# Performance work log

Measured on AMD Instinct MI355X. Metric: run time of the kernel, lower is better.

Reference implementation:

```python
import jax, jax.numpy as jnp
import numpy as np

B, P, E = 64, 196, 2048      # batch, num_pixels (14*14), encoder_size
H, EMB, V = 512, 512, 10000  # hidden_size, embed_size, vocab_size
T_CAP = 50                   # hard-coded pred/alpha buffer length
T_MAX = T_CAP - 1            # max(decode_lengths) = max(lengths) - 1 = 49


def setup_inputs() -> dict:
    key = jax.random.key(0)
    ks = jax.random.split(key, 20)

    def lin(k, out_f, in_f):
        kw, kb = jax.random.split(k)
        s = 1.0 / np.sqrt(in_f)
        return (jax.random.uniform(kw, (out_f, in_f), jnp.float32, -s, s),
                jax.random.uniform(kb, (out_f,), jnp.float32, -s, s))

    features = jax.random.normal(ks[0], (B, P, E), jnp.float32)
    captions = jax.random.randint(ks[1], (B, T_CAP), 0, V)
    # sorted descending, first length forced to 50 so max(decode_lengths)=49
    lengths = jnp.sort(jax.random.randint(ks[2], (B,), 2, T_CAP + 1))[::-1]
    lengths = lengths.at[0].set(T_CAP)

    Wx_w, Wx_b = lin(ks[3], E, E)          # attention Wx: encoder->encoder
    Wh_w, Wh_b = lin(ks[4], E, H)          # attention Wh: hidden->encoder
    V_w, V_b = lin(ks[5], 1, E)            # attention V: encoder->1
    init_h_w, init_h_b = lin(ks[6], H, E)  # init_h
    f_beta_w, f_beta_b = lin(ks[7], E, H)  # f_beta gate
    embed_w = jax.random.normal(ks[8], (V, EMB), jnp.float32)
    gru_w_ih, gru_b_ih = lin(ks[9], 3 * H, E + EMB)
    gru_w_hh, gru_b_hh = lin(ks[10], 3 * H, H)
    fc1_w, fc1_b = lin(ks[11], V, H)

    return dict(features=features, captions=captions, lengths=lengths,
                Wx_w=Wx_w, Wx_b=Wx_b, Wh_w=Wh_w, Wh_b=Wh_b, V_w=V_w, V_b=V_b,
                init_h_w=init_h_w, init_h_b=init_h_b,
                f_beta_w=f_beta_w, f_beta_b=f_beta_b, embed_w=embed_w,
                gru_w_ih=gru_w_ih, gru_b_ih=gru_b_ih,
                gru_w_hh=gru_w_hh, gru_b_hh=gru_b_hh,
                fc1_w=fc1_w, fc1_b=fc1_b)


def reference(features, captions, lengths, Wx_w, Wx_b, Wh_w, Wh_b, V_w, V_b,
              init_h_w, init_h_b, f_beta_w, f_beta_b, embed_w,
              gru_w_ih, gru_b_ih, gru_w_hh, gru_b_hh, fc1_w, fc1_b):
    b, p, e = features.shape
    vsz = fc1_w.shape[0]
    dec = lengths - 1                                  # decode_lengths
    # init hidden state from mean-pooled features
    h0 = jnp.mean(features, axis=1) @ init_h_w.T + init_h_b      # [B,H]
    # Wx(features) is time-invariant: precompute once
    x_wx = jnp.einsum('bpe,fe->bpf', features, Wx_w) + Wx_b      # [B,P,E]
    emb = embed_w[captions]                                      # [B,50,EMB]
    emb_t = jnp.transpose(emb[:, :T_MAX], (1, 0, 2))             # [T,B,EMB]

    def step(h, xs):
        t, e_t = xs
        active = (dec >= t)                            # rows still decoding
        # Bahdanau attention
        h_wh = h @ Wh_w.T + Wh_b                       # [B,E]
        lam = jnp.einsum('bpe,oe->bpo',
                         jnp.tanh(x_wx + h_wh[:, None, :]), V_w) + V_b
        alpha = jax.nn.softmax(lam, axis=1)            # [B,P,1]
        z = jnp.sum(alpha * features, axis=1)          # [B,E]
        # sigmoid gate
        gate = jax.nn.sigmoid(h @ f_beta_w.T + f_beta_b)
        inp = jnp.concatenate([gate * z, e_t], axis=1)  # [B,E+EMB]
        # GRUCell (torch gate order r,z,n)
        gi = inp @ gru_w_ih.T + gru_b_ih
        gh = h @ gru_w_hh.T + gru_b_hh
        i_r, i_z, i_n = jnp.split(gi, 3, axis=-1)
        h_r, h_z, h_n = jnp.split(gh, 3, axis=-1)
        r = jax.nn.sigmoid(i_r + h_r)
        zg = jax.nn.sigmoid(i_z + h_z)
        n = jnp.tanh(i_n + r * h_n)
        h_new = (1.0 - zg) * n + zg * h
        pred = h_new @ fc1_w.T + fc1_b                 # dropout in eval = id
        m = active[:, None]
        h_out = jnp.where(m, h_new, h)                 # freeze finished rows
        return h_out, (jnp.where(m, pred, 0.0),
                       jnp.where(m, alpha[..., 0], 0.0))

    _, (preds_t, alphas_t) = jax.lax.scan(
        step, h0, (jnp.arange(T_MAX), emb_t))
    preds = jnp.zeros((b, T_CAP, vsz), features.dtype)
    preds = preds.at[:, :T_MAX].set(jnp.transpose(preds_t, (1, 0, 2)))
    alphas = jnp.zeros((b, T_CAP, p), features.dtype)
    alphas = alphas.at[:, :T_MAX].set(jnp.transpose(alphas_t, (1, 0, 2)))
    return preds, alphas, dec
```

## Files before the change

### kernel.cpp

```cpp
#include <hip/hip_runtime.h>
#include <cstddef>

#define B_    64
#define P_    196
#define E_    2048
#define H_    512
#define EMB_  512
#define V_    10000
#define TCAP_ 50
#define TMAX_ 49
#define KI_   2560
#define G3_   1536
#define NBLK_ 512
#define FSTRIDE 32
#define COLLECTOR_ (NBLK_ - 1)

typedef __attribute__((ext_vector_type(8))) short short8;
typedef __attribute__((ext_vector_type(4))) float floatx4;
typedef unsigned int u32;
typedef __attribute__((ext_vector_type(4))) unsigned int u32x4;
typedef const __attribute__((address_space(1))) u32* gptr_t;
typedef __attribute__((address_space(3))) u32* lptr_t;

__device__ __forceinline__ unsigned short f2bf_rne(float f) {
    unsigned int x = __float_as_uint(f);
    unsigned int r = (x + 0x7fffu + ((x >> 16) & 1u)) >> 16;
    return (unsigned short)r;
}
__device__ __forceinline__ float bf2f(unsigned int u16) {
    return __uint_as_float(u16 << 16);
}
__device__ __forceinline__ float fast_tanh(float x) {
    float a = fabsf(x);
    float e = __expf(2.0f * a);
    float r = 1.0f - 2.0f / (e + 1.0f);
    return (x < 0.0f) ? -r : r;
}
__device__ __forceinline__ float fast_sig(float x) {
    return 1.0f / (1.0f + __expf(-x));
}

__device__ __forceinline__ float ldf(const float* p) {
    return __hip_atomic_load((float*)p, __ATOMIC_RELAXED, __HIP_MEMORY_SCOPE_AGENT);
}
__device__ __forceinline__ void stf(float* p, float v) {
    __hip_atomic_store(p, v, __ATOMIC_RELAXED, __HIP_MEMORY_SCOPE_AGENT);
}
__device__ __forceinline__ void stu(u32* p, u32 v) {
    __hip_atomic_store(p, v, __ATOMIC_RELAXED, __HIP_MEMORY_SCOPE_AGENT);
}
__device__ __forceinline__ short8 cvt8(u32x4 v) {
    union { u32x4 u; short8 s; } x; x.u = v; return x.s;
}

#define GLD16(dst, base, OFF) \
    asm volatile("global_load_dwordx4 %0, %1, off offset:" #OFF " sc1" \
                 : "=v"(dst) : "v"(base) : "memory")

__device__ __forceinline__ void gbar(unsigned int* __restrict__ flags,
                                     unsigned int* __restrict__ go,
                                     unsigned int ep)
{
    asm volatile("s_waitcnt vmcnt(0)" ::: "memory");
    __syncthreads();
    if (blockIdx.x == COLLECTOR_) {
        int tid = threadIdx.x;
        for (int s = tid; s < NBLK_ - 1; s += 256) {
            while (__hip_atomic_load(&flags[s * FSTRIDE], __ATOMIC_RELAXED,
                                     __HIP_MEMORY_SCOPE_AGENT) < ep)
                __builtin_amdgcn_s_sleep(1);
        }
        __syncthreads();
        if (tid < 8)
            __hip_atomic_store(&go[tid * FSTRIDE], ep, __ATOMIC_RELAXED,
                               __HIP_MEMORY_SCOPE_AGENT);
    } else {
        if (threadIdx.x == 0) {
            __hip_atomic_store(&flags[blockIdx.x * FSTRIDE], ep, __ATOMIC_RELAXED,
                               __HIP_MEMORY_SCOPE_AGENT);
            while (__hip_atomic_load(&go[(blockIdx.x & 7) * FSTRIDE], __ATOMIC_RELAXED,
                                     __HIP_MEMORY_SCOPE_AGENT) < ep)
                __builtin_amdgcn_s_sleep(2);
        }
    }
    __syncthreads();
}

__global__ void init_out_kernel(float* __restrict__ preds, float* __restrict__ alphas,
                                float* __restrict__ dec, const int* __restrict__ lens,
                                unsigned int* __restrict__ flags, unsigned int* __restrict__ go)
{
    int i = blockIdx.x * 256 + threadIdx.x;
    if (i < NBLK_ * FSTRIDE) flags[i] = 0u;
    if (i < 8 * FSTRIDE) go[i] = 0u;
    if (i < B_ * V_) {
        int b = i / V_, v = i - b * V_;
        preds[((size_t)b * TCAP_ + TMAX_) * V_ + v] = 0.f;
    }
    if (i < B_ * P_) {
        int b = i / P_, p = i - b * P_;
        alphas[((size_t)b * TCAP_ + TMAX_) * P_ + p] = 0.f;
    }
    if (i < B_) dec[i] = (float)(lens[i] - 1);
}

__global__ void f2bf_kernel(const float* __restrict__ src, unsigned short* __restrict__ dst, int n8)
{
    int i = blockIdx.x * 256 + threadIdx.x;
    if (i >= n8) return;
    float4 a = ((const float4*)src)[2 * i];
    float4 b = ((const float4*)src)[2 * i + 1];
    uint4 o;
    o.x = (unsigned)f2bf_rne(a.x) | ((unsigned)f2bf_rne(a.y) << 16);
    o.y = (unsigned)f2bf_rne(a.z) | ((unsigned)f2bf_rne(a.w) << 16);
    o.z = (unsigned)f2bf_rne(b.x) | ((unsigned)f2bf_rne(b.y) << 16);
    o.w = (unsigned)f2bf_rne(b.z) | ((unsigned)f2bf_rne(b.w) << 16);
    ((uint4*)dst)[i] = o;
}

__global__ void mean_kernel(const float* __restrict__ f, unsigned short* __restrict__ out)
{
    int i = blockIdx.x * 256 + threadIdx.x;
    int b = i >> 11, e = i & 2047;
    const float* p = f + (size_t)b * P_ * E_ + e;
    float s = 0.f;
    #pragma unroll 4
    for (int k = 0; k < P_; ++k) s += p[(size_t)k * E_];
    out[i] = f2bf_rne(s * (1.0f / (float)P_));
}

__global__ void __launch_bounds__(256)
mfma_xwx_kernel(const unsigned short* __restrict__ A,
                const unsigned short* __restrict__ W,
                const float* __restrict__ bias,
                unsigned short* __restrict__ C)
{
    __shared__ unsigned short As[128 * 64];
    __shared__ unsigned short Bs[128 * 64];
    int wv = threadIdx.x >> 6, lane = threadIdx.x & 63;
    int mr = lane & 15, quad = lane >> 4;
    int m0 = blockIdx.y * 128;
    int n0 = blockIdx.x * 128;
    int wm = (wv & 1) * 64, wn = (wv >> 1) * 64;
    int srow = wv * 32;
    int lrow = lane >> 3;
    int lcol = (lane & 7) * 8;
    floatx4 acc[4][4] = {};
    for (int k0 = 0; k0 < E_; k0 += 64) {
        __syncthreads();
        #pragma unroll
        for (int i = 0; i < 4; ++i) {
            int r = srow + i * 8;
            __builtin_amdgcn_global_load_lds(
                (gptr_t)(A + (size_t)(m0 + r + lrow) * E_ + k0 + lcol),
                (lptr_t)(As + r * 64), 16, 0, 0);
            __builtin_amdgcn_global_load_lds(
                (gptr_t)(W + (size_t)(n0 + r + lrow) * E_ + k0 + lcol),
                (lptr_t)(Bs + r * 64), 16, 0, 0);
        }
        __syncthreads();
        #pragma unroll
        for (int kk = 0; kk < 64; kk += 32) {
            short8 af[4], bf[4];
            #pragma unroll
            for (int i = 0; i < 4; ++i)
                af[i] = *(const short8*)(As + (wm + i * 16 + mr) * 64 + kk + quad * 8);
            #pragma unroll
            for (int j = 0; j < 4; ++j)
                bf[j] = *(const short8*)(Bs + (wn + j * 16 + mr) * 64 + kk + quad * 8);
            #pragma unroll
            for (int i = 0; i < 4; ++i)
                #pragma unroll
                for (int j = 0; j < 4; ++j)
                    acc[i][j] = __builtin_amdgcn_mfma_f32_16x16x32_bf16(af[i], bf[j], acc[i][j], 0, 0, 0);
        }
    }
    #pragma unroll
    for (int j = 0; j < 4; ++j) {
        int col = n0 + wn + j * 16 + mr;
        float bs = bias[col];
        #pragma unroll
        for (int i = 0; i < 4; ++i) {
            int row = m0 + wm + i * 16 + quad * 4;
            #pragma unroll
            for (int ii = 0; ii < 4; ++ii)
                C[(size_t)(row + ii) * E_ + col] = f2bf_rne(acc[i][j][ii] + bs);
        }
    }
}

__global__ void __launch_bounds__(256)
fc1tile_kernel(const unsigned short* __restrict__ Hall,
               const unsigned short* __restrict__ W,
               const float* __restrict__ bias,
               float* __restrict__ preds, const int* __restrict__ lens)
{
    __shared__ unsigned short As[128 * 64];
    __shared__ unsigned short Bs[128 * 64];
    int wv = threadIdx.x >> 6, lane = threadIdx.x & 63;
    int mr = lane & 15, quad = lane >> 4;
    int m0 = blockIdx.y * 128;
    int n0 = blockIdx.x * 128;
    int wm = (wv & 1) * 64, wn = (wv >> 1) * 64;
    int srow = wv * 32;
    int lrow = lane >> 3;
    int lcol = (lane & 7) * 8;
    floatx4 acc[4][4] = {};
    for (int k0 = 0; k0 < H_; k0 += 64) {
        __syncthreads();
        #pragma unroll
        for (int i = 0; i < 4; ++i) {
            int r = srow + i * 8;
            __builtin_amdgcn_global_load_lds(
                (gptr_t)(Hall + (size_t)(m0 + r + lrow) * H_ + k0 + lcol),
                (lptr_t)(As + r * 64), 16, 0, 0);
            __builtin_amdgcn_global_load_lds(
                (gptr_t)(W + (size_t)(n0 + r + lrow) * H_ + k0 + lcol),
                (lptr_t)(Bs + r * 64), 16, 0, 0);
        }
        __syncthreads();
        #pragma unroll
        for (int kk = 0; kk < 64; kk += 32) {
            short8 af[4], bf[4];
            #pragma unroll
            for (int i = 0; i < 4; ++i)
                af[i] = *(const short8*)(As + (wm + i * 16 + mr) * 64 + kk + quad * 8);
            #pragma unroll
            for (int j = 0; j < 4; ++j)
                bf[j] = *(const short8*)(Bs + (wn + j * 16 + mr) * 64 + kk + quad * 8);
            #pragma unroll
            for (int i = 0; i < 4; ++i)
                #pragma unroll
                for (int j = 0; j < 4; ++j)
                    acc[i][j] = __builtin_amdgcn_mfma_f32_16x16x32_bf16(af[i], bf[j], acc[i][j], 0, 0, 0);
        }
    }
    #pragma unroll
    for (int j = 0; j < 4; ++j) {
        int col = n0 + wn + j * 16 + mr;
        float bs = bias[min(col, V_ - 1)];
        #pragma unroll
        for (int i = 0; i < 4; ++i) {
            int row = m0 + wm + i * 16 + quad * 4;
            #pragma unroll
            for (int ii = 0; ii < 4; ++ii) {
                int r = row + ii;
                if (r < TMAX_ * B_ && col < V_) {
                    int t = r >> 6, b = r & 63;
                    float v = (lens[b] > t) ? (acc[i][j][ii] + bs) : 0.f;
                    preds[((size_t)b * TCAP_ + t) * V_ + col] = v;
                }
            }
        }
    }
}

template<int KC>
__global__ void __launch_bounds__(256)
mfma_gemm64(const unsigned short* __restrict__ A, int ld,
            const unsigned short* __restrict__ W,
            const float* __restrict__ bias,
            float* __restrict__ C, unsigned short* __restrict__ Cbf, int ldc)
{
    int wv = threadIdx.x >> 6, lane = threadIdx.x & 63;
    int mr = lane & 15, quad = lane >> 4;
    int m0 = wv * 16;
    int n0 = blockIdx.x * 16;
    const unsigned short* pa = A + (size_t)(m0 + mr) * ld + quad * 8;
    const unsigned short* pb = W + (size_t)(n0 + mr) * ld + quad * 8;
    floatx4 acc = {0.f, 0.f, 0.f, 0.f};
    #pragma unroll 16
    for (int k0 = 0; k0 < KC; k0 += 32) {
        short8 a = *(const short8*)(const void*)(pa + k0);
        short8 b = *(const short8*)(const void*)(pb + k0);
        acc = __builtin_amdgcn_mfma_f32_16x16x32_bf16(a, b, acc, 0, 0, 0);
    }
    int col = n0 + mr;
    float bs = bias ? bias[col] : 0.f;
    #pragma unroll
    for (int i = 0; i < 4; ++i) {
        int row = m0 + quad * 4 + i;
        float v = acc[i] + bs;
        C[(size_t)row * ldc + col] = v;
        if (Cbf) Cbf[(size_t)row * ldc + col] = f2bf_rne(v);
    }
}

__global__ void __launch_bounds__(256, 2)
loop_kernel(unsigned short* __restrict__ hbf,
            const unsigned short* __restrict__ whbf, const float* __restrict__ Wh_b,
            const unsigned short* __restrict__ fbbf, const float* __restrict__ fb_b,
            const unsigned short* __restrict__ ghhbf, const float* __restrict__ ghh_b,
            float* __restrict__ hwh, float* __restrict__ hf, float* __restrict__ gh,
            const unsigned short* __restrict__ xwx,
            const float* __restrict__ Vw, const float* __restrict__ Vb,
            float* __restrict__ lam,
            const unsigned short* __restrict__ fbf,
            const float* __restrict__ embed_w,
            const int* __restrict__ captions, const int* __restrict__ lens,
            unsigned short* __restrict__ inpbf,
            float* __restrict__ alphas,
            const unsigned short* __restrict__ wihbf, const float* __restrict__ b_ih,
            const float* __restrict__ h0,
            unsigned short* __restrict__ Hall,
            unsigned int* __restrict__ flags, unsigned int* __restrict__ go)
{
    __shared__ float smem[5376];
    float* sv = smem + 3328;
    const int bid = blockIdx.x;
    const int tid = threadIdx.x;
    const int wv = tid >> 6, lane = tid & 63;
    const int mr = lane & 15, quad = lane >> 4;
    unsigned int ep = 0;

    {
        const float4* vs = (const float4*)Vw;
        ((float4*)sv)[tid]       = vs[tid];
        ((float4*)sv)[tid + 256] = vs[tid + 256];
    }

    float hreg = 0.f;
    if (bid < 128) {
        int row = tid >> 4, col = tid & 15;
        int b = (bid >> 5) * 16 + row, j = (bid & 31) * 16 + col;
        hreg = h0[(size_t)b * H_ + j];
    }

    for (int t = 0; t < TMAX_; ++t) {
        if (bid < 352) {
            const unsigned short* W; const float* bias; float* C; int n0; int ldc;
            if (bid < 128)      { W = whbf;  bias = Wh_b;  C = hwh; n0 = bid * 16;         ldc = E_; }
            else if (bid < 256) { W = fbbf;  bias = fb_b;  C = hf;  n0 = (bid - 128) * 16; ldc = E_; }
            else                { W = ghhbf; bias = ghh_b; C = gh;  n0 = (bid - 256) * 16; ldc = G3_; }
            int m0 = wv * 16;
            const unsigned short* pa = hbf + (size_t)(m0 + mr) * H_ + quad * 8;
            const unsigned short* pb = W + (size_t)(n0 + mr) * H_ + quad * 8;
            u32x4 av[16];
            GLD16(av[0],  pa, 0);    GLD16(av[1],  pa, 64);
            GLD16(av[2],  pa, 128);  GLD16(av[3],  pa, 192);
            GLD16(av[4],  pa, 256);  GLD16(av[5],  pa, 320);
            GLD16(av[6],  pa, 384);  GLD16(av[7],  pa, 448);
            GLD16(av[8],  pa, 512);  GLD16(av[9],  pa, 576);
            GLD16(av[10], pa, 640);  GLD16(av[11], pa, 704);
            GLD16(av[12], pa, 768);  GLD16(av[13], pa, 832);
            GLD16(av[14], pa, 896);  GLD16(av[15], pa, 960);
            asm volatile("s_waitcnt vmcnt(0)"
                : "+v"(av[0]), "+v"(av[1]), "+v"(av[2]),  "+v"(av[3]),
                  "+v"(av[4]), "+v"(av[5]), "+v"(av[6]),  "+v"(av[7]),
                  "+v"(av[8]), "+v"(av[9]), "+v"(av[10]), "+v"(av[11]),
                  "+v"(av[12]),"+v"(av[13]),"+v"(av[14]), "+v"(av[15])
                :: "memory");
            __builtin_amdgcn_sched_barrier(0);
            floatx4 acc0 = {0.f, 0.f, 0.f, 0.f};
            floatx4 acc1 = {0.f, 0.f, 0.f, 0.f};
            #pragma unroll
            for (int i = 0; i < 16; i += 2) {
                short8 b0 = *(const short8*)(const void*)(pb + i * 32);
                short8 b1 = *(const short8*)(const void*)(pb + i * 32 + 32);
                acc0 = __builtin_amdgcn_mfma_f32_16x16x32_bf16(cvt8(av[i]),     b0, acc0, 0, 0, 0);
                acc1 = __builtin_amdgcn_mfma_f32_16x16x32_bf16(cvt8(av[i + 1]), b1, acc1, 0, 0, 0);
            }
            floatx4 acc = acc0 + acc1;
            int col = n0 + mr;
            float bs = bias[col];
            #pragma unroll
            for (int i = 0; i < 4; ++i)
                stf(&C[(size_t)(m0 + quad * 4 + i) * ldc + col], acc[i] + bs);
        }
        gbar(flags, go, ++ep);

        {
            int b = bid >> 3, q = bid & 7;
            float* sh = smem;
            const float* hsrc = hwh + (size_t)b * E_;
            u32x4 hv0, hv1;
            GLD16(hv0, hsrc + tid * 4, 0);
            GLD16(hv1, hsrc + 1024 + tid * 4, 0);
            asm volatile("s_waitcnt vmcnt(0)" : "+v"(hv0), "+v"(hv1) :: "memory");
            __builtin_amdgcn_sched_barrier(0);
            ((u32x4*)sh)[tid]       = hv0;
            ((u32x4*)sh)[tid + 256] = hv1;
            __syncthreads();
            float vb0 = Vb[0];
            #pragma unroll
            for (int i = 0; i < 7; ++i) {
                int pl = wv + i * 4;
                int p = q * 25 + pl;
                if (pl < 25 && p < P_) {
                    const unsigned short* px = xwx + ((size_t)b * P_ + p) * E_;
                    float acc = 0.f;
                    #pragma unroll
                    for (int it = 0; it < 4; ++it) {
                        int e = it * 512 + lane * 8;
                        u32x4 u = *(const u32x4*)(const void*)(px + e);
                        float4 h0v = *(const float4*)(sh + e);
                        float4 h1v = *(const float4*)(sh + e + 4);
                        float4 v0 = *(const float4*)(sv + e);
                        float4 v1 = *(const float4*)(sv + e + 4);
                        acc = fmaf(fast_tanh(bf2f(u[0] & 0xffffu) + h0v.x), v0.x, acc);
                        acc = fmaf(fast_tanh(bf2f(u[0] >> 16)     + h0v.y), v0.y, acc);
                        acc = fmaf(fast_tanh(bf2f(u[1] & 0xffffu) + h0v.z), v0.z, acc);
                        acc = fmaf(fast_tanh(bf2f(u[1] >> 16)     + h0v.w), v0.w, acc);
                        acc = fmaf(fast_tanh(bf2f(u[2] & 0xffffu) + h1v.x), v1.x, acc);
                        acc = fmaf(fast_tanh(bf2f(u[2] >> 16)     + h1v.y), v1.y, acc);
                        acc = fmaf(fast_tanh(bf2f(u[3] & 0xffffu) + h1v.z), v1.z, acc);
                        acc = fmaf(fast_tanh(bf2f(u[3] >> 16)     + h1v.w), v1.w, acc);
                    }
                    #pragma unroll
                    for (int off = 32; off > 0; off >>= 1) acc += __shfl_down(acc, off);
                    if (lane == 0) stf(&lam[b * P_ + p], acc + vb0);
                }
            }
        }
        gbar(flags, go, ++ep);

        {
            int b = bid >> 3, c = bid & 7;
            int e0 = c * 256;
            float* sa = smem;
            float* sr = smem + 256;
            float* ps = smem + 512;
            float x = (tid < P_) ? ldf(&lam[b * P_ + tid]) : -1e30f;
            float mxl = x;
            #pragma unroll
            for (int off = 32; off > 0; off >>= 1) mxl = fmaxf(mxl, __shfl_xor(mxl, off));
            if (lane == 0) sr[wv] = mxl;
            __syncthreads();
            float mx = fmaxf(fmaxf(sr[0], sr[1]), fmaxf(sr[2], sr[3]));
            float ex = (tid < P_) ? __expf(x - mx) : 0.f;
            sa[tid] = ex;
            float sml = ex;
            #pragma unroll
            for (int off = 32; off > 0; off >>= 1) sml += __shfl_xor(sml, off);
            if (lane == 0) sr[4 + wv] = sml;
            __syncthreads();
            float inv = 1.f / (sr[4] + sr[5] + sr[6] + sr[7]);
            if (c == 0 && tid < P_)
                alphas[(size_t)b * TCAP_ * P_ + (size_t)t * P_ + tid] = (lens[b] > t) ? ex * inv : 0.f;
            if (c == 1) {
                int cap = captions[b * TCAP_ + t];
                float2 v = *(const float2*)(embed_w + (size_t)cap * EMB_ + tid * 2);
                stu((u32*)(inpbf + (size_t)b * KI_ + E_) + tid,
                    (u32)f2bf_rne(v.x) | ((u32)f2bf_rne(v.y) << 16));
            }
            int half = tid >> 7, li = tid & 127;
            const unsigned short* fp = fbf + ((size_t)b * P_ + half) * E_ + e0 + li * 2;
            float a0 = 0.f, a1 = 0.f;
            #pragma unroll 7
            for (int p = half; p < P_; p += 2) {
                u32 u = *(const u32*)(const void*)fp;
                fp += 2 * E_;
                float wgt = sa[p];
                a0 = fmaf(wgt, bf2f(u & 0xffffu), a0);
                a1 = fmaf(wgt, bf2f(u >> 16), a1);
            }
            ps[tid * 2]     = a0;
            ps[tid * 2 + 1] = a1;
            __syncthreads();
            if (tid < 128) {
                float z0 = (ps[tid * 2]     + ps[(tid + 128) * 2])     * inv;
                float z1 = (ps[tid * 2 + 1] + ps[(tid + 128) * 2 + 1]) * inv;
                float g0 = ldf(hf + (size_t)b * E_ + e0 + tid * 2);
                float g1 = ldf(hf + (size_t)b * E_ + e0 + tid * 2 + 1);
                stu((u32*)(inpbf + (size_t)b * KI_ + e0) + tid,
                    (u32)f2bf_rne(fast_sig(g0) * z0) | ((u32)f2bf_rne(fast_sig(g1) * z1) << 16));
            }
        }
        gbar(flags, go, ++ep);

        if (bid < 128) {
            float (*red)[3][16][17] = (float (*)[3][16][17])smem;
            int j0 = (bid & 31) * 16;
            int m0 = (bid >> 5) * 16;
            int koff = wv * 640;
            const unsigned short* pa  = inpbf + (size_t)(m0 + mr) * KI_ + koff + quad * 8;
            const unsigned short* pb0 = wihbf + (size_t)(j0 + mr) * KI_ + koff + quad * 8;
            const unsigned short* pb1 = pb0 + (size_t)512 * KI_;
            const unsigned short* pb2 = pb0 + (size_t)1024 * KI_;
            u32x4 av[20];
            GLD16(av[0],  pa, 0);     GLD16(av[1],  pa, 64);
            GLD16(av[2],  pa, 128);   GLD16(av[3],  pa, 192);
            GLD16(av[4],  pa, 256);   GLD16(av[5],  pa, 320);
            GLD16(av[6],  pa, 384);   GLD16(av[7],  pa, 448);
            GLD16(av[8],  pa, 512);   GLD16(av[9],  pa, 576);
            GLD16(av[10], pa, 640);   GLD16(av[11], pa, 704);
            GLD16(av[12], pa, 768);   GLD16(av[13], pa, 832);
            GLD16(av[14], pa, 896);   GLD16(av[15], pa, 960);
            GLD16(av[16], pa, 1024);  GLD16(av[17], pa, 1088);
            GLD16(av[18], pa, 1152);  GLD16(av[19], pa, 1216);
            asm volatile("s_waitcnt vmcnt(0)"
                : "+v"(av[0]), "+v"(av[1]), "+v"(av[2]),  "+v"(av[3]),
                  "+v"(av[4]), "+v"(av[5]), "+v"(av[6]),  "+v"(av[7]),
                  "+v"(av[8]), "+v"(av[9]), "+v"(av[10]), "+v"(av[11]),
                  "+v"(av[12]),"+v"(av[13]),"+v"(av[14]), "+v"(av[15]),
                  "+v"(av[16]),"+v"(av[17]),"+v"(av[18]), "+v"(av[19])
                :: "memory");
            __builtin_amdgcn_sched_barrier(0);
            floatx4 ar = {0.f,0.f,0.f,0.f}, az = {0.f,0.f,0.f,0.f}, an = {0.f,0.f,0.f,0.f};
            #pragma unroll
            for (int k = 0; k < 20; ++k) {
                short8 a  = cvt8(av[k]);
                short8 br = *(const short8*)(const void*)(pb0 + k * 32);
                short8 bz = *(const short8*)(const void*)(pb1 + k * 32);
                short8 bn = *(const short8*)(const void*)(pb2 + k * 32);
                ar = __builtin_amdgcn_mfma_f32_16x16x32_bf16(a, br, ar, 0, 0, 0);
                az = __builtin_amdgcn_mfma_f32_16x16x32_bf16(a, bz, az, 0, 0, 0);
                an = __builtin_amdgcn_mfma_f32_16x16x32_bf16(a, bn, an, 0, 0, 0);
            }
            #pragma unroll
            for (int i = 0; i < 4; ++i) {
                red[wv][0][quad * 4 + i][mr] = ar[i];
                red[wv][1][quad * 4 + i][mr] = az[i];
                red[wv][2][quad * 4 + i][mr] = an[i];
            }
            __syncthreads();
            int row = tid >> 4, col = tid & 15;
            int b = m0 + row, j = j0 + col;
            float ir = red[0][0][row][col] + red[1][0][row][col] + red[2][0][row][col] + red[3][0][row][col] + b_ih[j];
            float iz = red[0][1][row][col] + red[1][1][row][col] + red[2][1][row][col] + red[3][1][row][col] + b_ih[512 + j];
            float in_= red[0][2][row][col] + red[1][2][row][col] + red[2][2][row][col] + red[3][2][row][col] + b_ih[1024 + j];
            float hr = ldf(&gh[(size_t)b * G3_ + j]);
            float hz = ldf(&gh[(size_t)b * G3_ + 512 + j]);
            float hn = ldf(&gh[(size_t)b * G3_ + 1024 + j]);
            float r  = fast_sig(ir + hr);
            float zg = fast_sig(iz + hz);
            float n  = fast_tanh(in_ + r * hn);
            float hv = (1.f - zg) * n + zg * hreg;
            float ho = (lens[b] > t) ? hv : hreg;
            hreg = ho;
            unsigned short hob = f2bf_rne(ho);
            u32 nb = (u32)(unsigned short)__shfl_down((int)hob, 1);
            if ((tid & 1) == 0)
                stu((u32*)hbf + ((size_t)b * H_ + j) / 2, (u32)hob | (nb << 16));
            Hall[((size_t)t * B_ + b) * H_ + j] = hob;
        }
        gbar(flags, go, ++ep);
    }
}

extern "C" void kernel_launch(void* const* d_in, const int* in_sizes, int n_in,
                              void* d_out, int out_size, void* d_ws, size_t ws_size,
                              hipStream_t stream)
{
    const float* features  = (const float*)d_in[0];
    const int*   captions  = (const int*)d_in[1];
    const int*   lengths   = (const int*)d_in[2];
    const float* Wx_w      = (const float*)d_in[3];
    const float* Wx_b      = (const float*)d_in[4];
    const float* Wh_w      = (const float*)d_in[5];
    const float* Wh_b      = (const float*)d_in[6];
    const float* V_w       = (const float*)d_in[7];
    const float* V_b       = (const float*)d_in[8];
    const float* init_h_w  = (const float*)d_in[9];
    const float* init_h_b  = (const float*)d_in[10];
    const float* f_beta_w  = (const float*)d_in[11];
    const float* f_beta_b  = (const float*)d_in[12];
    const float* embed_w   = (const float*)d_in[13];
    const float* gru_w_ih  = (const float*)d_in[14];
    const float* gru_b_ih  = (const float*)d_in[15];
    const float* gru_w_hh  = (const float*)d_in[16];
    const float* gru_b_hh  = (const float*)d_in[17];
    const float* fc1_w     = (const float*)d_in[18];
    const float* fc1_b     = (const float*)d_in[19];

    float* preds  = (float*)d_out;
    float* alphas = preds + (size_t)B_ * TCAP_ * V_;
    float* dec    = alphas + (size_t)B_ * TCAP_ * P_;

    char* w = (char*)d_ws;
    unsigned short* fbf     = (unsigned short*)w; w += (size_t)12544 * 2048 * 2;
    unsigned short* xwx     = (unsigned short*)w; w += (size_t)12544 * 2048 * 2;
    unsigned short* wxbf    = (unsigned short*)w; w += (size_t)2048 * 2048 * 2;
    unsigned short* whbf    = (unsigned short*)w; w += (size_t)2048 * 512 * 2;
    unsigned short* fbbf    = (unsigned short*)w; w += (size_t)2048 * 512 * 2;
    unsigned short* ghhbf   = (unsigned short*)w; w += (size_t)1536 * 512 * 2;
    unsigned short* wihbf   = (unsigned short*)w; w += (size_t)1536 * 2560 * 2;
    unsigned short* fc1bf   = (unsigned short*)w; w += (size_t)10112 * 512 * 2;
    unsigned short* ihwbf   = (unsigned short*)w; w += (size_t)512 * 2048 * 2;
    unsigned short* fmeanbf = (unsigned short*)w; w += (size_t)64 * 2048 * 2;
    unsigned short* hbf     = (unsigned short*)w; w += (size_t)64 * 512 * 2;
    unsigned short* inpbf   = (unsigned short*)w; w += (size_t)64 * KI_ * 2;
    unsigned short* Hall    = (unsigned short*)w; w += (size_t)3200 * 512 * 2;
    float* h   = (float*)w; w += (size_t)64 * 512 * 4;
    float* hwh = (float*)w; w += (size_t)64 * 2048 * 4;
    float* hf  = (float*)w; w += (size_t)64 * 2048 * 4;
    float* gh  = (float*)w; w += (size_t)64 * 1536 * 4;
    float* lam = (float*)w; w += (size_t)64 * 196 * 4;
    unsigned int* flags = (unsigned int*)w; w += (size_t)NBLK_ * FSTRIDE * 4;
    unsigned int* go    = (unsigned int*)w; w += (size_t)8 * FSTRIDE * 4;

    init_out_kernel<<<2500, 256, 0, stream>>>(preds, alphas, dec, lengths, flags, go);

    f2bf_kernel<<<12544, 256, 0, stream>>>(features, fbf, 12544 * 2048 / 8);
    f2bf_kernel<<<2048, 256, 0, stream>>>(Wx_w, wxbf, 2048 * 2048 / 8);
    f2bf_kernel<<<512, 256, 0, stream>>>(Wh_w, whbf, 2048 * 512 / 8);
    f2bf_kernel<<<512, 256, 0, stream>>>(f_beta_w, fbbf, 2048 * 512 / 8);
    f2bf_kernel<<<384, 256, 0, stream>>>(gru_w_hh, ghhbf, 1536 * 512 / 8);
    f2bf_kernel<<<1920, 256, 0, stream>>>(gru_w_ih, wihbf, 1536 * 2560 / 8);
    f2bf_kernel<<<2500, 256, 0, stream>>>(fc1_w, fc1bf, 10000 * 512 / 8);
    f2bf_kernel<<<512, 256, 0, stream>>>(init_h_w, ihwbf, 512 * 2048 / 8);

    mean_kernel<<<512, 256, 0, stream>>>(features, fmeanbf);
    mfma_gemm64<2048><<<32, 256, 0, stream>>>(fmeanbf, 2048, ihwbf, init_h_b, h, hbf, 512);
    mfma_xwx_kernel<<<dim3(16, 98), 256, 0, stream>>>(fbf, wxbf, Wx_b, xwx);

    loop_kernel<<<NBLK_, 256, 0, stream>>>(hbf, whbf, Wh_b, fbbf, f_beta_b, ghhbf, gru_b_hh,
                                           hwh, hf, gh, xwx, V_w, V_b, lam, fbf, embed_w,
                                           captions, lengths, inpbf, alphas, wihbf, gru_b_ih,
                                           h, Hall, flags, go);

    fc1tile_kernel<<<dim3(79, 25), 256, 0, stream>>>(Hall, fc1bf, fc1_b, preds, lengths);
}
```

Before: 3.646 ms.

## Double persistent grid to 1024 blocks and split register-staged loads in halves

Raises the persistent loop kernel's grid from 512 to 1024 blocks with four blocks per CU, and adds more go flags for the grid barrier. The attention-score and context phases now give each batch row 16 blocks instead of 8, with the context reduction using 8 row groups and 4-wide loads. The hidden-state and GRU input GEMMs now load their A operands in two halves of registers instead of one batch to reduce VGPR pressure enough for the higher occupancy. In exchange the grid barrier has to wait on twice as many blocks each phase, and each half-load waits on its own vmcnt(0), which adds latency.

```diff
diff --git a/kernel.cpp b/kernel.cpp
--- a/kernel.cpp
+++ b/kernel.cpp
@@ -11,13 +11,15 @@
 #define TMAX_ 49
 #define KI_   2560
 #define G3_   1536
-#define NBLK_ 512
+#define NBLK_ 1024
 #define FSTRIDE 32
+#define NGO_  16
 #define COLLECTOR_ (NBLK_ - 1)
 
 typedef __attribute__((ext_vector_type(8))) short short8;
 typedef __attribute__((ext_vector_type(4))) float floatx4;
 typedef unsigned int u32;
+typedef __attribute__((ext_vector_type(2))) unsigned int u32x2;
 typedef __attribute__((ext_vector_type(4))) unsigned int u32x4;
 typedef const __attribute__((address_space(1))) u32* gptr_t;
 typedef __attribute__((address_space(3))) u32* lptr_t;
@@ -71,15 +73,15 @@
                 __builtin_amdgcn_s_sleep(1);
         }
         __syncthreads();
-        if (tid < 8)
+        if (tid < NGO_)
             __hip_atomic_store(&go[tid * FSTRIDE], ep, __ATOMIC_RELAXED,
                                __HIP_MEMORY_SCOPE_AGENT);
     } else {
         if (threadIdx.x == 0) {
             __hip_atomic_store(&flags[blockIdx.x * FSTRIDE], ep, __ATOMIC_RELAXED,
                                __HIP_MEMORY_SCOPE_AGENT);
-            while (__hip_atomic_load(&go[(blockIdx.x & 7) * FSTRIDE], __ATOMIC_RELAXED,
-                                     __HIP_MEMORY_SCOPE_AGENT) < ep)
+            while (__hip_atomic_load(&go[(blockIdx.x & (NGO_ - 1)) * FSTRIDE],
+                                     __ATOMIC_RELAXED, __HIP_MEMORY_SCOPE_AGENT) < ep)
                 __builtin_amdgcn_s_sleep(2);
         }
     }
@@ -92,7 +94,7 @@
 {
     int i = blockIdx.x * 256 + threadIdx.x;
     if (i < NBLK_ * FSTRIDE) flags[i] = 0u;
-    if (i < 8 * FSTRIDE) go[i] = 0u;
+    if (i < NGO_ * FSTRIDE) go[i] = 0u;
     if (i < B_ * V_) {
         int b = i / V_, v = i - b * V_;
         preds[((size_t)b * TCAP_ + TMAX_) * V_ + v] = 0.f;
@@ -286,7 +288,7 @@
     }
 }
 
-__global__ void __launch_bounds__(256, 2)
+__global__ void __launch_bounds__(256, 4)
 loop_kernel(unsigned short* __restrict__ hbf,
             const unsigned short* __restrict__ whbf, const float* __restrict__ Wh_b,
             const unsigned short* __restrict__ fbbf, const float* __restrict__ fb_b,
@@ -335,31 +337,39 @@
             int m0 = wv * 16;
             const unsigned short* pa = hbf + (size_t)(m0 + mr) * H_ + quad * 8;
             const unsigned short* pb = W + (size_t)(n0 + mr) * H_ + quad * 8;
-            u32x4 av[16];
-            GLD16(av[0],  pa, 0);    GLD16(av[1],  pa, 64);
-            GLD16(av[2],  pa, 128);  GLD16(av[3],  pa, 192);
-            GLD16(av[4],  pa, 256);  GLD16(av[5],  pa, 320);
-            GLD16(av[6],  pa, 384);  GLD16(av[7],  pa, 448);
-            GLD16(av[8],  pa, 512);  GLD16(av[9],  pa, 576);
-            GLD16(av[10], pa, 640);  GLD16(av[11], pa, 704);
-            GLD16(av[12], pa, 768);  GLD16(av[13], pa, 832);
-            GLD16(av[14], pa, 896);  GLD16(av[15], pa, 960);
-            asm volatile("s_waitcnt vmcnt(0)"
-                : "+v"(av[0]), "+v"(av[1]), "+v"(av[2]),  "+v"(av[3]),
-                  "+v"(av[4]), "+v"(av[5]), "+v"(av[6]),  "+v"(av[7]),
-                  "+v"(av[8]), "+v"(av[9]), "+v"(av[10]), "+v"(av[11]),
-                  "+v"(av[12]),"+v"(av[13]),"+v"(av[14]), "+v"(av[15])
-                :: "memory");
-            __builtin_amdgcn_sched_barrier(0);
+            u32x4 av[8];
             floatx4 acc0 = {0.f, 0.f, 0.f, 0.f};
             floatx4 acc1 = {0.f, 0.f, 0.f, 0.f};
-            #pragma unroll
-            for (int i = 0; i < 16; i += 2) {
+            GLD16(av[0], pa, 0);    GLD16(av[1], pa, 64);
+            GLD16(av[2], pa, 128);  GLD16(av[3], pa, 192);
+            GLD16(av[4], pa, 256);  GLD16(av[5], pa, 320);
+            GLD16(av[6], pa, 384);  GLD16(av[7], pa, 448);
+            asm volatile("s_waitcnt vmcnt(0)"
+                : "+v"(av[0]), "+v"(av[1]), "+v"(av[2]), "+v"(av[3]),
+                  "+v"(av[4]), "+v"(av[5]), "+v"(av[6]), "+v"(av[7]) :: "memory");
+            __builtin_amdgcn_sched_barrier(0);
+            #pragma unroll
+            for (int i = 0; i < 8; i += 2) {
                 short8 b0 = *(const short8*)(const void*)(pb + i * 32);
                 short8 b1 = *(const short8*)(const void*)(pb + i * 32 + 32);
                 acc0 = __builtin_amdgcn_mfma_f32_16x16x32_bf16(cvt8(av[i]),     b0, acc0, 0, 0, 0);
                 acc1 = __builtin_amdgcn_mfma_f32_16x16x32_bf16(cvt8(av[i + 1]), b1, acc1, 0, 0, 0);
             }
+            GLD16(av[0], pa, 512);  GLD16(av[1], pa, 576);
+            GLD16(av[2], pa, 640);  GLD16(av[3], pa, 704);
+            GLD16(av[4], pa, 768);  GLD16(av[5], pa, 832);
+            GLD16(av[6], pa, 896);  GLD16(av[7], pa, 960);
+            asm volatile("s_waitcnt vmcnt(0)"
+                : "+v"(av[0]), "+v"(av[1]), "+v"(av[2]), "+v"(av[3]),
+                  "+v"(av[4]), "+v"(av[5]), "+v"(av[6]), "+v"(av[7]) :: "memory");
+            __builtin_amdgcn_sched_barrier(0);
+            #pragma unroll
+            for (int i = 0; i < 8; i += 2) {
+                short8 b0 = *(const short8*)(const void*)(pb + 256 + i * 32);
+                short8 b1 = *(const short8*)(const void*)(pb + 256 + i * 32 + 32);
+                acc0 = __builtin_amdgcn_mfma_f32_16x16x32_bf16(cvt8(av[i]),     b0, acc0, 0, 0, 0);
+                acc1 = __builtin_amdgcn_mfma_f32_16x16x32_bf16(cvt8(av[i + 1]), b1, acc1, 0, 0, 0);
+            }
             floatx4 acc = acc0 + acc1;
             int col = n0 + mr;
             float bs = bias[col];
@@ -370,7 +380,7 @@
         gbar(flags, go, ++ep);
 
         {
-            int b = bid >> 3, q = bid & 7;
+            int b = bid >> 4, q = bid & 15;
             float* sh = smem;
             const float* hsrc = hwh + (size_t)b * E_;
             u32x4 hv0, hv1;
@@ -383,10 +393,10 @@
             __syncthreads();
             float vb0 = Vb[0];
             #pragma unroll
-            for (int i = 0; i < 7; ++i) {
+            for (int i = 0; i < 4; ++i) {
                 int pl = wv + i * 4;
-                int p = q * 25 + pl;
-                if (pl < 25 && p < P_) {
+                int p = q + pl * 16;
+                if (pl < 13 && p < P_) {
                     const unsigned short* px = xwx + ((size_t)b * P_ + p) * E_;
                     float acc = 0.f;
                     #pragma unroll
@@ -415,8 +425,8 @@
         gbar(flags, go, ++ep);
 
         {
-            int b = bid >> 3, c = bid & 7;
-            int e0 = c * 256;
+            int b = bid >> 4, c = bid & 15;
+            int e0 = c * 128;
             float* sa = smem;
             float* sr = smem + 256;
             float* ps = smem + 512;
@@ -443,25 +453,33 @@
                 stu((u32*)(inpbf + (size_t)b * KI_ + E_) + tid,
                     (u32)f2bf_rne(v.x) | ((u32)f2bf_rne(v.y) << 16));
             }
-            int half = tid >> 7, li = tid & 127;
-            const unsigned short* fp = fbf + ((size_t)b * P_ + half) * E_ + e0 + li * 2;
-            float a0 = 0.f, a1 = 0.f;
-            #pragma unroll 7
-            for (int p = half; p < P_; p += 2) {
-                u32 u = *(const u32*)(const void*)fp;
-                fp += 2 * E_;
+            int rg = tid >> 5;
+            int cl = (tid & 31) * 4;
+            const unsigned short* fp = fbf + ((size_t)b * P_ + rg) * E_ + e0 + cl;
+            float a0 = 0.f, a1 = 0.f, a2 = 0.f, a3 = 0.f;
+            for (int p = rg; p < P_; p += 8) {
+                u32x2 u = *(const u32x2*)(const void*)fp;
+                fp += (size_t)8 * E_;
                 float wgt = sa[p];
-                a0 = fmaf(wgt, bf2f(u & 0xffffu), a0);
-                a1 = fmaf(wgt, bf2f(u >> 16), a1);
-            }
-            ps[tid * 2]     = a0;
-            ps[tid * 2 + 1] = a1;
+                a0 = fmaf(wgt, bf2f(u[0] & 0xffffu), a0);
+                a1 = fmaf(wgt, bf2f(u[0] >> 16),     a1);
+                a2 = fmaf(wgt, bf2f(u[1] & 0xffffu), a2);
+                a3 = fmaf(wgt, bf2f(u[1] >> 16),     a3);
+            }
+            float* pw = ps + rg * 128 + cl;
+            pw[0] = a0; pw[1] = a1; pw[2] = a2; pw[3] = a3;
             __syncthreads();
-            if (tid < 128) {
-                float z0 = (ps[tid * 2]     + ps[(tid + 128) * 2])     * inv;
-                float z1 = (ps[tid * 2 + 1] + ps[(tid + 128) * 2 + 1]) * inv;
-                float g0 = ldf(hf + (size_t)b * E_ + e0 + tid * 2);
-                float g1 = ldf(hf + (size_t)b * E_ + e0 + tid * 2 + 1);
+            if (tid < 64) {
+                int col = tid * 2;
+                float z0 = 0.f, z1 = 0.f;
+                #pragma unroll
+                for (int r8 = 0; r8 < 8; ++r8) {
+                    z0 += ps[r8 * 128 + col];
+                    z1 += ps[r8 * 128 + col + 1];
+                }
+                z0 *= inv; z1 *= inv;
+                float g0 = ldf(hf + (size_t)b * E_ + e0 + col);
+                float g1 = ldf(hf + (size_t)b * E_ + e0 + col + 1);
                 stu((u32*)(inpbf + (size_t)b * KI_ + e0) + tid,
                     (u32)f2bf_rne(fast_sig(g0) * z0) | ((u32)f2bf_rne(fast_sig(g1) * z1) << 16));
             }
@@ -477,32 +495,44 @@
             const unsigned short* pb0 = wihbf + (size_t)(j0 + mr) * KI_ + koff + quad * 8;
             const unsigned short* pb1 = pb0 + (size_t)512 * KI_;
             const unsigned short* pb2 = pb0 + (size_t)1024 * KI_;
-            u32x4 av[20];
-            GLD16(av[0],  pa, 0);     GLD16(av[1],  pa, 64);
-            GLD16(av[2],  pa, 128);   GLD16(av[3],  pa, 192);
-            GLD16(av[4],  pa, 256);   GLD16(av[5],  pa, 320);
-            GLD16(av[6],  pa, 384);   GLD16(av[7],  pa, 448);
-            GLD16(av[8],  pa, 512);   GLD16(av[9],  pa, 576);
-            GLD16(av[10], pa, 640);   GLD16(av[11], pa, 704);
-            GLD16(av[12], pa, 768);   GLD16(av[13], pa, 832);
-            GLD16(av[14], pa, 896);   GLD16(av[15], pa, 960);
-            GLD16(av[16], pa, 1024);  GLD16(av[17], pa, 1088);
-            GLD16(av[18], pa, 1152);  GLD16(av[19], pa, 1216);
+            floatx4 ar = {0.f,0.f,0.f,0.f}, az = {0.f,0.f,0.f,0.f}, an = {0.f,0.f,0.f,0.f};
+            u32x4 av[10];
+            GLD16(av[0], pa, 0);    GLD16(av[1], pa, 64);
+            GLD16(av[2], pa, 128);  GLD16(av[3], pa, 192);
+            GLD16(av[4], pa, 256);  GLD16(av[5], pa, 320);
+            GLD16(av[6], pa, 384);  GLD16(av[7], pa, 448);
+            GLD16(av[8], pa, 512);  GLD16(av[9], pa, 576);
             asm volatile("s_waitcnt vmcnt(0)"
-                : "+v"(av[0]), "+v"(av[1]), "+v"(av[2]),  "+v"(av[3]),
-                  "+v"(av[4]), "+v"(av[5]), "+v"(av[6]),  "+v"(av[7]),
-                  "+v"(av[8]), "+v"(av[9]), "+v"(av[10]), "+v"(av[11]),
-                  "+v"(av[12]),"+v"(av[13]),"+v"(av[14]), "+v"(av[15]),
-                  "+v"(av[16]),"+v"(av[17]),"+v"(av[18]), "+v"(av[19])
+                : "+v"(av[0]), "+v"(av[1]), "+v"(av[2]), "+v"(av[3]), "+v"(av[4]),
+                  "+v"(av[5]), "+v"(av[6]), "+v"(av[7]), "+v"(av[8]), "+v"(av[9])
                 :: "memory");
             __builtin_amdgcn_sched_barrier(0);
-            floatx4 ar = {0.f,0.f,0.f,0.f}, az = {0.f,0.f,0.f,0.f}, an = {0.f,0.f,0.f,0.f};
-            #pragma unroll
-            for (int k = 0; k < 20; ++k) {
+            #pragma unroll
+            for (int k = 0; k < 10; ++k) {
                 short8 a  = cvt8(av[k]);
                 short8 br = *(const short8*)(const void*)(pb0 + k * 32);
                 short8 bz = *(const short8*)(const void*)(pb1 + k * 32);
                 short8 bn = *(const short8*)(const void*)(pb2 + k * 32);
+                ar = __builtin_amdgcn_mfma_f32_16x16x32_bf16(a, br, ar, 0, 0, 0);
+                az = __builtin_amdgcn_mfma_f32_16x16x32_bf16(a, bz, az, 0, 0, 0);
+                an = __builtin_amdgcn_mfma_f32_16x16x32_bf16(a, bn, an, 0, 0, 0);
+            }
+            GLD16(av[0], pa, 640);  GLD16(av[1], pa, 704);
+            GLD16(av[2], pa, 768);  GLD16(av[3], pa, 832);
+            GLD16(av[4], pa, 896);  GLD16(av[5], pa, 960);
+            GLD16(av[6], pa, 1024); GLD16(av[7], pa, 1088);
+            GLD16(av[8], pa, 1152); GLD16(av[9], pa, 1216);
+            asm volatile("s_waitcnt vmcnt(0)"
+                : "+v"(av[0]), "+v"(av[1]), "+v"(av[2]), "+v"(av[3]), "+v"(av[4]),
+                  "+v"(av[5]), "+v"(av[6]), "+v"(av[7]), "+v"(av[8]), "+v"(av[9])
+                :: "memory");
+            __builtin_amdgcn_sched_barrier(0);
+            #pragma unroll
+            for (int k = 0; k < 10; ++k) {
+                short8 a  = cvt8(av[k]);
+                short8 br = *(const short8*)(const void*)(pb0 + 320 + k * 32);
+                short8 bz = *(const short8*)(const void*)(pb1 + 320 + k * 32);
+                short8 bn = *(const short8*)(const void*)(pb2 + 320 + k * 32);
                 ar = __builtin_amdgcn_mfma_f32_16x16x32_bf16(a, br, ar, 0, 0, 0);
                 az = __builtin_amdgcn_mfma_f32_16x16x32_bf16(a, bz, az, 0, 0, 0);
                 an = __builtin_amdgcn_mfma_f32_16x16x32_bf16(a, bn, an, 0, 0, 0);
@@ -587,7 +617,7 @@
     float* gh  = (float*)w; w += (size_t)64 * 1536 * 4;
     float* lam = (float*)w; w += (size_t)64 * 196 * 4;
     unsigned int* flags = (unsigned int*)w; w += (size_t)NBLK_ * FSTRIDE * 4;
-    unsigned int* go    = (unsigned int*)w; w += (size_t)8 * FSTRIDE * 4;
+    unsigned int* go    = (unsigned int*)w; w += (size_t)NGO_ * FSTRIDE * 4;
 
     init_out_kernel<<<2500, 256, 0, stream>>>(preds, alphas, dec, lengths, flags, go);
 
```

After: 4.054 ms. 11.2% more time.
